# Kernel optimization log

Measured on AMD Instinct MI355X. Metric: run time of the kernel, lower is better.

Reference implementation:

```python
import jax, jax.numpy as jnp
import numpy as np

N_NODES = 50000
N_EDGES = 800000
N_FEAT = 128
N_HID = 256
N_PAIRS = 100000


def _gcn_norm(edge_index, n_nodes):
    # add self loops, compute D^-1/2 (A+I) D^-1/2 edge weights (PyG gcn_norm)
    loops = jnp.arange(n_nodes, dtype=edge_index.dtype)
    row = jnp.concatenate([edge_index[0], loops])
    col = jnp.concatenate([edge_index[1], loops])
    deg = jax.ops.segment_sum(jnp.ones_like(col, dtype=jnp.float32), col,
                              num_segments=n_nodes)
    dinv = jnp.where(deg > 0, jax.lax.rsqrt(deg), 0.0)
    norm = dinv[row] * dinv[col]  # [E + N]
    return row, col, norm


def _gcn_conv(x, W, b, row, col, norm, n_nodes):
    h = x @ W                       # [N, out]
    msg = h[row] * norm[:, None]    # gather + scale  [E+N, out]
    agg = jax.ops.segment_sum(msg, col, num_segments=n_nodes)  # scatter-add
    return agg + b


def setup_inputs() -> dict:
    key = jax.random.key(0)
    ks = jax.random.split(key, 9)
    edge_index = jax.random.randint(ks[0], (2, N_EDGES), 0, N_NODES, dtype=jnp.int64)
    features = jax.random.normal(ks[1], (N_NODES, N_FEAT), dtype=jnp.float32)
    mask = jax.random.randint(ks[2], (N_PAIRS, 2), 0, N_NODES, dtype=jnp.int64)
    s1 = 1.0 / np.sqrt(N_FEAT)
    s2 = 1.0 / np.sqrt(N_HID)
    W1 = jax.random.uniform(ks[3], (N_FEAT, N_HID), jnp.float32, -s1, s1)
    b1 = jnp.zeros((N_HID,), jnp.float32)
    W2 = jax.random.uniform(ks[4], (N_HID, N_FEAT), jnp.float32, -s2, s2)
    b2 = jnp.zeros((N_FEAT,), jnp.float32)
    Wl = jax.random.uniform(ks[5], (N_HID, 1), jnp.float32, -s2, s2)
    bl = jax.random.uniform(ks[6], (1,), jnp.float32, -s2, s2)
    return {"edge_index": edge_index, "features": features, "mask": mask,
            "W1": W1, "b1": b1, "W2": W2, "b2": b2, "Wl": Wl, "bl": bl}


def reference(edge_index, features, mask, W1, b1, W2, b2, Wl, bl):
    n = features.shape[0]
    row, col, norm = _gcn_norm(edge_index, n)
    h = _gcn_conv(features, W1, b1, row, col, norm, n)   # GCNConv a
    h = jax.nn.relu(h)                                   # dropout p=0 -> identity
    h = _gcn_conv(h, W2, b2, row, col, norm, n)          # GCNConv b
    mt = mask.T
    p1 = jax.lax.stop_gradient(h[mt[0]])                 # .detach()
    p2 = jax.lax.stop_gradient(h[mt[1]])
    hp = jnp.concatenate([p1, p2], axis=1)               # [n_pairs, 2*n_feat]
    return jax.nn.sigmoid(hp @ Wl + bl)
```

## Files before the change

### kernel.cpp

```cpp
#include <hip/hip_runtime.h>
#include <math.h>

#define NFEAT 128
#define NHID 256
#define NBLK 128

typedef __attribute__((ext_vector_type(8))) short short8;
typedef __attribute__((ext_vector_type(4))) float f32x4;

__device__ inline unsigned short f2bf(float f) {
  unsigned u = __float_as_uint(f);
  u += 0x7fffu + ((u >> 16) & 1u);
  return (unsigned short)(u >> 16);
}
__device__ inline float bflo(unsigned u) { return __uint_as_float(u << 16); }
__device__ inline float bfhi(unsigned u) { return __uint_as_float(u & 0xffff0000u); }


__device__ inline void packOne(const float* __restrict__ W,
                               unsigned short* __restrict__ Wp, int idx, int KS,
                               int OUT) {
  int lane = idx & 63;
  int t = idx >> 6;
  int ks = t % KS;
  int nt = t / KS;
  int n = nt * 16 + (lane & 15);
  int k0 = ks * 32 + (lane >> 4) * 8;
  unsigned short v[8];
#pragma unroll
  for (int j = 0; j < 8; j++) v[j] = f2bf(W[(size_t)(k0 + j) * OUT + n]);
  *reinterpret_cast<short8*>(Wp + (size_t)idx * 8) =
      *reinterpret_cast<short8*>(v);
}

__global__ __launch_bounds__(1024) void k_hist_pack(
    const int* __restrict__ col, int* __restrict__ hist2d, int nE, int nb,
    const float* __restrict__ W1, const float* __restrict__ W2,
    unsigned short* __restrict__ W1p, unsigned short* __restrict__ W2p) {
  if (blockIdx.x >= NBLK) {
    int idx = (blockIdx.x - NBLK) * 1024 + threadIdx.x;
    if (idx < 4096) packOne(W1, W1p, idx, 4, 256);
    else packOne(W2, W2p, idx - 4096, 8, 128);
    return;
  }
  __shared__ int h[1024];
  for (int i = threadIdx.x; i < nb; i += 1024) h[i] = 0;
  __syncthreads();
  int chunk = (nE + NBLK - 1) / NBLK;
  int beg = blockIdx.x * chunk, end = min(beg + chunk, nE);
  for (int e = beg + threadIdx.x; e < end; e += 1024)
    atomicAdd(&h[col[e] >> 6], 1);
  __syncthreads();
  for (int i = threadIdx.x; i < nb; i += 1024)
    hist2d[i * NBLK + blockIdx.x] = h[i];
}

__global__ __launch_bounds__(256) void k_bsum(const int* __restrict__ a,
                                              int* __restrict__ psum, int S,
                                              const float* __restrict__ b2,
                                              const float* __restrict__ Wl,
                                              const float* __restrict__ bl,
                                              float* __restrict__ Cbuf) {
  int t = threadIdx.x;
  if (blockIdx.x == gridDim.x - 1) {
    float v = (t < 128) ? b2[t] * (Wl[t] + Wl[128 + t]) : 0.f;
#pragma unroll
    for (int o = 32; o; o >>= 1) v += __shfl_down(v, o);
    __shared__ float fw[4];
    if ((t & 63) == 0) fw[t >> 6] = v;
    __syncthreads();
    if (t == 0) Cbuf[0] = fw[0] + fw[1] + fw[2] + fw[3] + bl[0];
    return;
  }
  int i = blockIdx.x * 256 + t;
  int v = (i < S) ? a[i] : 0;
#pragma unroll
  for (int o = 32; o; o >>= 1) v += __shfl_down(v, o);
  __shared__ int ws[4];
  if ((t & 63) == 0) ws[t >> 6] = v;
  __syncthreads();
  if (t == 0) psum[blockIdx.x] = ws[0] + ws[1] + ws[2] + ws[3];
}

__global__ __launch_bounds__(256) void k_s3m(const int* __restrict__ a,
                                             const int* __restrict__ psum,
                                             int* __restrict__ out, int S) {
  __shared__ int sh[256];
  __shared__ int ws[4];
  int t = threadIdx.x;
  int b = blockIdx.x;
  int partial = 0;
  for (int i = t; i < b; i += 256) partial += psum[i];
#pragma unroll
  for (int o = 32; o; o >>= 1) partial += __shfl_down(partial, o);
  if ((t & 63) == 0) ws[t >> 6] = partial;
  int i = b * 256 + t;
  int d = (i < S) ? a[i] : 0;
  sh[t] = d;
  __syncthreads();
  int base = ws[0] + ws[1] + ws[2] + ws[3];
  for (int o = 1; o < 256; o <<= 1) {
    int u = (t >= o) ? sh[t - o] : 0;
    __syncthreads();
    sh[t] += u;
    __syncthreads();
  }
  if (i < S) out[i] = base + sh[t] - d;
}

__global__ __launch_bounds__(1024) void k_part2(const int* __restrict__ row,
                                                const int* __restrict__ col,
                                                const int* __restrict__ sbase,
                                                unsigned* __restrict__ tmp,
                                                int nE, int nb) {
  __shared__ int cur[1024];
  for (int i = threadIdx.x; i < nb; i += 1024)
    cur[i] = sbase[i * NBLK + blockIdx.x];
  __syncthreads();
  int chunk = (nE + NBLK - 1) / NBLK;
  int beg = blockIdx.x * chunk, end = min(beg + chunk, nE);
  for (int e = beg + threadIdx.x; e < end; e += 1024) {
    int c = col[e];
    int pos = atomicAdd(&cur[c >> 6], 1);
    tmp[pos] = ((unsigned)(c & 63) << 16) | (unsigned)row[e];
  }
}

__global__ __launch_bounds__(256) void k_bsort_cvt(
    const unsigned* __restrict__ tmp, const int* __restrict__ sbase,
    int* __restrict__ ebuf, int* __restrict__ offs, float* __restrict__ dinv,
    const float* __restrict__ feat, unsigned short* __restrict__ xs, int n,
    int nE, int nb) {
  __shared__ int bins[64], cur[64];
  __shared__ float sdinv[64];
  int b = blockIdx.x;
  int beg = sbase[b * NBLK];
  int end = (b == nb - 1) ? nE : sbase[(b + 1) * NBLK];
  int t = threadIdx.x;
  if (t == 0 && b == nb - 1) offs[n] = nE;
  if (t < 64) bins[t] = 0;
  __syncthreads();
  for (int i = beg + t; i < end; i += 256) atomicAdd(&bins[tmp[i] >> 16], 1);
  __syncthreads();
  if (t < 64) {
    int v = bins[t];
    int s = v;
#pragma unroll
    for (int o = 1; o < 64; o <<= 1) {
      int u = __shfl_up(s, o);
      if (t >= o) s += u;
    }
    int off = beg + s - v;
    cur[t] = off;
    float dv = rsqrtf((float)(v + 1));
    sdinv[t] = dv;
    int node = b * 64 + t;
    if (node < n) {
      offs[node] = off;
      dinv[node] = dv;
    }
  }
  __syncthreads();
  for (int i = beg + t; i < end; i += 256) {
    unsigned p = tmp[i];
    int pos = atomicAdd(&cur[p >> 16], 1);
    ebuf[pos] = (int)(p & 0xffffu);
  }
  for (int i = t; i < 64 * 32; i += 256) {
    int r = i >> 5;
    int node = b * 64 + r;
    if (node >= n) break;
    float d = sdinv[r];
    float4 v = reinterpret_cast<const float4*>(feat)[(size_t)node * 32 + (i & 31)];
    unsigned short o[4] = {f2bf(v.x * d), f2bf(v.y * d), f2bf(v.z * d),
                           f2bf(v.w * d)};
    reinterpret_cast<ushort4*>(xs)[(size_t)node * 32 + (i & 31)] =
        *reinterpret_cast<ushort4*>(o);
  }
}

__global__ __launch_bounds__(256) void k_agg_bf(
    const unsigned int* __restrict__ G, const int* __restrict__ offs,
    const int* __restrict__ ebuf, const float* __restrict__ dinv,
    unsigned int* __restrict__ OUTP, int n) {
  int node = blockIdx.x * 4 + (threadIdx.x >> 6);
  if (node >= n) return;
  int lane = threadIdx.x & 63;
  int g = lane >> 4;
  int c = lane & 15;
  int beg = offs[node], end = offs[node + 1];
  float acc[8];
  if (g == 0) {
    uint4 s = *reinterpret_cast<const uint4*>(G + (size_t)node * 64 + c * 4);
    acc[0] = bflo(s.x); acc[1] = bfhi(s.x); acc[2] = bflo(s.y); acc[3] = bfhi(s.y);
    acc[4] = bflo(s.z); acc[5] = bfhi(s.z); acc[6] = bflo(s.w); acc[7] = bfhi(s.w);
  } else {
#pragma unroll
    for (int j = 0; j < 8; j++) acc[j] = 0.f;
  }
  int e = beg + g;
  for (; e + 4 < end; e += 8) {
    int i0 = ebuf[e], i1 = ebuf[e + 4];
    uint4 v0 = *reinterpret_cast<const uint4*>(G + (size_t)i0 * 64 + c * 4);
    uint4 v1 = *reinterpret_cast<const uint4*>(G + (size_t)i1 * 64 + c * 4);
    acc[0] += bflo(v0.x); acc[1] += bfhi(v0.x);
    acc[2] += bflo(v0.y); acc[3] += bfhi(v0.y);
    acc[4] += bflo(v0.z); acc[5] += bfhi(v0.z);
    acc[6] += bflo(v0.w); acc[7] += bfhi(v0.w);
    acc[0] += bflo(v1.x); acc[1] += bfhi(v1.x);
    acc[2] += bflo(v1.y); acc[3] += bfhi(v1.y);
    acc[4] += bflo(v1.z); acc[5] += bfhi(v1.z);
    acc[6] += bflo(v1.w); acc[7] += bfhi(v1.w);
  }
  if (e < end) {
    uint4 v = *reinterpret_cast<const uint4*>(G + (size_t)ebuf[e] * 64 + c * 4);
    acc[0] += bflo(v.x); acc[1] += bfhi(v.x);
    acc[2] += bflo(v.y); acc[3] += bfhi(v.y);
    acc[4] += bflo(v.z); acc[5] += bfhi(v.z);
    acc[6] += bflo(v.w); acc[7] += bfhi(v.w);
  }
#pragma unroll
  for (int j = 0; j < 8; j++) {
    acc[j] += __shfl_down(acc[j], 32);
    acc[j] += __shfl_down(acc[j], 16);
  }
  if (g == 0) {
    float d = dinv[node];
    unsigned o[4];
#pragma unroll
    for (int k = 0; k < 4; k++)
      o[k] = (unsigned)f2bf(acc[2 * k] * d) |
             ((unsigned)f2bf(acc[2 * k + 1] * d) << 16);
    *reinterpret_cast<uint4*>(OUTP + (size_t)node * 64 + c * 4) =
        *reinterpret_cast<uint4*>(o);
  }
}

__global__ __launch_bounds__(256) void k_mfma_fused(
    const unsigned short* __restrict__ A, const unsigned short* __restrict__ B1p,
    const unsigned short* __restrict__ B2p, const float* __restrict__ b1,
    const float* __restrict__ dinv, const float* __restrict__ Wl,
    float* __restrict__ P) {
  __shared__ unsigned short sh1[32 * 264];
  __shared__ float pacc[32][2];
  int rt0 = blockIdx.x * 2;
  int wave = threadIdx.x >> 6;
  int lane = threadIdx.x & 63;
  int quad = lane >> 4;
  int mrow0 = rt0 * 16 + (lane & 15);
  if (threadIdx.x < 64) pacc[threadIdx.x >> 1][threadIdx.x & 1] = 0.f;

  f32x4 acc[2][4] = {};
  const short8* Ap0 =
      reinterpret_cast<const short8*>(A + (size_t)mrow0 * NFEAT + quad * 8);
  const short8* Ap1 = reinterpret_cast<const short8*>(
      A + (size_t)(mrow0 + 16) * NFEAT + quad * 8);
#pragma unroll
  for (int ks = 0; ks < 4; ks++) {
    short8 a0 = Ap0[ks * 4];
    short8 a1 = Ap1[ks * 4];
#pragma unroll
    for (int ct = 0; ct < 4; ct++) {
      int nt = wave * 4 + ct;
      short8 b = *reinterpret_cast<const short8*>(
          B1p + ((size_t)(nt * 4 + ks) * 64 + lane) * 8);
      acc[0][ct] = __builtin_amdgcn_mfma_f32_16x16x32_bf16(a0, b, acc[0][ct], 0, 0, 0);
      acc[1][ct] = __builtin_amdgcn_mfma_f32_16x16x32_bf16(a1, b, acc[1][ct], 0, 0, 0);
    }
  }
#pragma unroll
  for (int ct = 0; ct < 4; ct++) {
    int c = (wave * 4 + ct) * 16 + (lane & 15);
    float bv = b1[c];
#pragma unroll
    for (int rg = 0; rg < 2; rg++)
#pragma unroll
      for (int i = 0; i < 4; i++) {
        float v = fmaxf(acc[rg][ct][i] + bv, 0.f);
        sh1[(rg * 16 + quad * 4 + i) * 264 + c] = f2bf(v);
      }
  }
  __syncthreads();

  f32x4 acc2[2][2] = {};
  const unsigned short* a2_0 = sh1 + (size_t)(lane & 15) * 264 + quad * 8;
  const unsigned short* a2_1 = sh1 + (size_t)(16 + (lane & 15)) * 264 + quad * 8;
#pragma unroll
  for (int ks = 0; ks < 8; ks++) {
    short8 a0 = *reinterpret_cast<const short8*>(a2_0 + ks * 32);
    short8 a1 = *reinterpret_cast<const short8*>(a2_1 + ks * 32);
#pragma unroll
    for (int ct = 0; ct < 2; ct++) {
      int nt = wave * 2 + ct;
      short8 b = *reinterpret_cast<const short8*>(
          B2p + ((size_t)(nt * 8 + ks) * 64 + lane) * 8);
      acc2[0][ct] = __builtin_amdgcn_mfma_f32_16x16x32_bf16(a0, b, acc2[0][ct], 0, 0, 0);
      acc2[1][ct] = __builtin_amdgcn_mfma_f32_16x16x32_bf16(a1, b, acc2[1][ct], 0, 0, 0);
    }
  }
  float p1[2][4] = {}, p2[2][4] = {};
#pragma unroll
  for (int rg = 0; rg < 2; rg++) {
    int r0 = (rt0 + rg) * 16 + quad * 4;
    float dv[4];
#pragma unroll
    for (int i = 0; i < 4; i++) dv[i] = dinv[r0 + i];
#pragma unroll
    for (int ct = 0; ct < 2; ct++) {
      int c = (wave * 2 + ct) * 16 + (lane & 15);
      float wl1 = Wl[c], wl2 = Wl[128 + c];
#pragma unroll
      for (int i = 0; i < 4; i++) {
        float v = acc2[rg][ct][i] * dv[i];
        p1[rg][i] = fmaf(v, wl1, p1[rg][i]);
        p2[rg][i] = fmaf(v, wl2, p2[rg][i]);
      }
    }
  }
#pragma unroll
  for (int rg = 0; rg < 2; rg++)
#pragma unroll
    for (int i = 0; i < 4; i++) {
#pragma unroll
      for (int o = 8; o; o >>= 1) {
        p1[rg][i] += __shfl_xor(p1[rg][i], o);
        p2[rg][i] += __shfl_xor(p2[rg][i], o);
      }
    }
  if ((lane & 15) == 0) {
#pragma unroll
    for (int rg = 0; rg < 2; rg++)
#pragma unroll
      for (int i = 0; i < 4; i++) {
        int row = rg * 16 + quad * 4 + i;
        atomicAdd(&pacc[row][0], p1[rg][i]);
        atomicAdd(&pacc[row][1], p2[rg][i]);
      }
  }
  __syncthreads();
  if (threadIdx.x < 64) {
    int row = threadIdx.x >> 1, comp = threadIdx.x & 1;
    P[(size_t)(rt0 * 16 + row) * 2 + comp] = pacc[row][comp];
  }
}

__global__ __launch_bounds__(256) void k_agg_s(const float2* __restrict__ p,
                                               const int* __restrict__ offs,
                                               const int* __restrict__ ebuf,
                                               const float* __restrict__ dinv,
                                               float2* __restrict__ q, int n) {
  int i = blockIdx.x * 256 + threadIdx.x;
  if (i >= n) return;
  int beg = offs[i], end = offs[i + 1];
  float2 s = p[i];
  int e = beg;
  for (; e + 4 <= end; e += 4) {
    int s0 = ebuf[e], s1 = ebuf[e + 1], s2 = ebuf[e + 2], s3 = ebuf[e + 3];
    float2 v0 = p[s0], v1 = p[s1], v2 = p[s2], v3 = p[s3];
    s.x += v0.x + v1.x + v2.x + v3.x;
    s.y += v0.y + v1.y + v2.y + v3.y;
  }
  for (; e < end; e++) {
    float2 v = p[ebuf[e]];
    s.x += v.x;
    s.y += v.y;
  }
  float d = dinv[i];
  q[i] = make_float2(s.x * d, s.y * d);
}

__global__ __launch_bounds__(256) void k_head2(const float2* __restrict__ q,
                                               const int* __restrict__ mask,
                                               const float* __restrict__ Cbuf,
                                               float* __restrict__ out, int P) {
  int p = blockIdx.x * 256 + threadIdx.x;
  if (p >= P) return;
  int m0 = mask[2 * p], m1 = mask[2 * p + 1];
  float s = q[m0].x + q[m1].y + Cbuf[0];
  out[p] = 1.0f / (1.0f + expf(-s));
}

extern "C" void kernel_launch(void* const* d_in, const int* in_sizes, int n_in,
                              void* d_out, int out_size, void* d_ws,
                              size_t ws_size, hipStream_t stream) {
  const int* edge = (const int*)d_in[0];
  const float* feat = (const float*)d_in[1];
  const int* mask = (const int*)d_in[2];
  const float* W1 = (const float*)d_in[3];
  const float* b1 = (const float*)d_in[4];
  const float* W2 = (const float*)d_in[5];
  const float* b2 = (const float*)d_in[6];
  const float* Wl = (const float*)d_in[7];
  const float* bl = (const float*)d_in[8];
  float* out = (float*)d_out;

  const int E = in_sizes[0] / 2;
  const int N = in_sizes[1] / NFEAT;
  const int P = in_sizes[2] / 2;
  const int* rowp = edge;
  const int* colp = edge + E;
  const int nrt = N / 16;
  const int nb = (N + 63) / 64;
  const int S = nb * NBLK;
  const int nS = (S + 255) / 256;

  auto aln = [](size_t x) { return (x + 255) & ~(size_t)255; };
  const size_t rowSlack = (size_t)16 * NFEAT * 2;
  char* w = (char*)d_ws;
  int* hist2d = (int*)w;           w += aln((size_t)S * 4);
  int* sbase = (int*)w;            w += aln((size_t)S * 4);
  int* psum = (int*)w;             w += aln((size_t)1024 * 4);
  float* Cbuf = (float*)w;         w += aln(256);
  int* offs = (int*)w;             w += aln((size_t)(N + 1) * 4);
  int* ebuf = (int*)w;             w += aln((size_t)E * 4);
  unsigned* tmp = (unsigned*)w;    w += aln((size_t)E * 4);
  float* dinv = (float*)w;         w += aln((size_t)N * 4 + 1024);
  unsigned short* xs = (unsigned short*)w;  w += aln((size_t)N * NFEAT * 2);
  unsigned short* z = (unsigned short*)w;   w += aln((size_t)N * NFEAT * 2 + rowSlack);
  float* p = (float*)w;            w += aln((size_t)(N + 32) * 8);
  float2* q = (float2*)w;          w += aln((size_t)N * 8);
  unsigned short* W1p = (unsigned short*)w; w += aln((size_t)NFEAT * NHID * 2);
  unsigned short* W2p = (unsigned short*)w; w += aln((size_t)NHID * NFEAT * 2);

  k_hist_pack<<<NBLK + 8, 1024, 0, stream>>>(colp, hist2d, E, nb, W1, W2, W1p,
                                             W2p);
  k_bsum<<<nS + 1, 256, 0, stream>>>(hist2d, psum, S, b2, Wl, bl, Cbuf);
  k_s3m<<<nS, 256, 0, stream>>>(hist2d, psum, sbase, S);
  k_part2<<<NBLK, 1024, 0, stream>>>(rowp, colp, sbase, tmp, E, nb);
  k_bsort_cvt<<<nb, 256, 0, stream>>>(tmp, sbase, ebuf, offs, dinv, feat, xs,
                                      N, E, nb);
  k_agg_bf<<<(N + 3) / 4, 256, 0, stream>>>((const unsigned*)xs, offs, ebuf,
                                            dinv, (unsigned*)z, N);
  k_mfma_fused<<<(nrt + 1) / 2, 256, 0, stream>>>(z, W1p, W2p, b1, dinv, Wl, p);
  k_agg_s<<<(N + 255) / 256, 256, 0, stream>>>((const float2*)p, offs, ebuf,
                                               dinv, q, N);
  k_head2<<<(P + 255) / 256, 256, 0, stream>>>(q, mask, Cbuf, out, P);
}
```

Baseline: 174.7 us.

## Slice feature matrix into column slabs for cache-friendly gather aggregation

The bf16 scaled feature matrix is stored as four 32-column slabs (slice-major), and the first aggregation kernel runs one grid per slab, so each gather touches a 64-byte row slice from a slab small enough to stay in cache. The aggregated output keeps the sliced layout, and the MFMA kernel reads its A operand from the slabs. Separately, the scalar second aggregation now uses four lanes per node with shuffle reduction instead of one thread per node, to balance degree variance. The cost is four times as many edge-index reads and more blocks, plus more shuffle reductions.

```diff
diff --git a/kernel.cpp b/kernel.cpp
--- a/kernel.cpp
+++ b/kernel.cpp
@@ -166,15 +166,18 @@
     int pos = atomicAdd(&cur[p >> 16], 1);
     ebuf[pos] = (int)(p & 0xffffu);
   }
-  for (int i = t; i < 64 * 32; i += 256) {
-    int r = i >> 5;
+  for (int i = t; i < 4 * 64 * 8; i += 256) {
+    int s = i >> 9;
+    int r = (i >> 3) & 63;
+    int ch = i & 7;
     int node = b * 64 + r;
-    if (node >= n) break;
+    if (node >= n) continue;
     float d = sdinv[r];
-    float4 v = reinterpret_cast<const float4*>(feat)[(size_t)node * 32 + (i & 31)];
+    float4 v =
+        reinterpret_cast<const float4*>(feat)[(size_t)node * 32 + s * 8 + ch];
     unsigned short o[4] = {f2bf(v.x * d), f2bf(v.y * d), f2bf(v.z * d),
                            f2bf(v.w * d)};
-    reinterpret_cast<ushort4*>(xs)[(size_t)node * 32 + (i & 31)] =
+    reinterpret_cast<ushort4*>(xs)[((size_t)s * n + node) * 8 + ch] =
         *reinterpret_cast<ushort4*>(o);
   }
 }
@@ -182,38 +185,26 @@
 __global__ __launch_bounds__(256) void k_agg_bf(
     const unsigned int* __restrict__ G, const int* __restrict__ offs,
     const int* __restrict__ ebuf, const float* __restrict__ dinv,
-    unsigned int* __restrict__ OUTP, int n) {
-  int node = blockIdx.x * 4 + (threadIdx.x >> 6);
+    unsigned int* __restrict__ OUTP, int n, int nbn, int zs) {
+  int slice = blockIdx.x / nbn;
+  int node = (blockIdx.x - slice * nbn) * 4 + (threadIdx.x >> 6);
   if (node >= n) return;
   int lane = threadIdx.x & 63;
-  int g = lane >> 4;
-  int c = lane & 15;
+  int g = lane >> 2;
+  int c = lane & 3;
   int beg = offs[node], end = offs[node + 1];
   float acc[8];
   if (g == 0) {
-    uint4 s = *reinterpret_cast<const uint4*>(G + (size_t)node * 64 + c * 4);
+    uint4 s = *reinterpret_cast<const uint4*>(G + ((size_t)slice * n + node) * 16 + c * 4);
     acc[0] = bflo(s.x); acc[1] = bfhi(s.x); acc[2] = bflo(s.y); acc[3] = bfhi(s.y);
     acc[4] = bflo(s.z); acc[5] = bfhi(s.z); acc[6] = bflo(s.w); acc[7] = bfhi(s.w);
   } else {
 #pragma unroll
     for (int j = 0; j < 8; j++) acc[j] = 0.f;
   }
-  int e = beg + g;
-  for (; e + 4 < end; e += 8) {
-    int i0 = ebuf[e], i1 = ebuf[e + 4];
-    uint4 v0 = *reinterpret_cast<const uint4*>(G + (size_t)i0 * 64 + c * 4);
-    uint4 v1 = *reinterpret_cast<const uint4*>(G + (size_t)i1 * 64 + c * 4);
-    acc[0] += bflo(v0.x); acc[1] += bfhi(v0.x);
-    acc[2] += bflo(v0.y); acc[3] += bfhi(v0.y);
-    acc[4] += bflo(v0.z); acc[5] += bfhi(v0.z);
-    acc[6] += bflo(v0.w); acc[7] += bfhi(v0.w);
-    acc[0] += bflo(v1.x); acc[1] += bfhi(v1.x);
-    acc[2] += bflo(v1.y); acc[3] += bfhi(v1.y);
-    acc[4] += bflo(v1.z); acc[5] += bfhi(v1.z);
-    acc[6] += bflo(v1.w); acc[7] += bfhi(v1.w);
-  }
-  if (e < end) {
-    uint4 v = *reinterpret_cast<const uint4*>(G + (size_t)ebuf[e] * 64 + c * 4);
+  for (int e = beg + g; e < end; e += 16) {
+    int src = ebuf[e];
+    uint4 v = *reinterpret_cast<const uint4*>(G + ((size_t)slice * n + src) * 16 + c * 4);
     acc[0] += bflo(v.x); acc[1] += bfhi(v.x);
     acc[2] += bflo(v.y); acc[3] += bfhi(v.y);
     acc[4] += bflo(v.z); acc[5] += bfhi(v.z);
@@ -223,6 +214,8 @@
   for (int j = 0; j < 8; j++) {
     acc[j] += __shfl_down(acc[j], 32);
     acc[j] += __shfl_down(acc[j], 16);
+    acc[j] += __shfl_down(acc[j], 8);
+    acc[j] += __shfl_down(acc[j], 4);
   }
   if (g == 0) {
     float d = dinv[node];
@@ -231,7 +224,7 @@
     for (int k = 0; k < 4; k++)
       o[k] = (unsigned)f2bf(acc[2 * k] * d) |
              ((unsigned)f2bf(acc[2 * k + 1] * d) << 16);
-    *reinterpret_cast<uint4*>(OUTP + (size_t)node * 64 + c * 4) =
+    *reinterpret_cast<uint4*>(OUTP + ((size_t)slice * zs + node) * 16 + c * 4) =
         *reinterpret_cast<uint4*>(o);
   }
 }
@@ -240,7 +233,7 @@
     const unsigned short* __restrict__ A, const unsigned short* __restrict__ B1p,
     const unsigned short* __restrict__ B2p, const float* __restrict__ b1,
     const float* __restrict__ dinv, const float* __restrict__ Wl,
-    float* __restrict__ P) {
+    float* __restrict__ P, int zs) {
   __shared__ unsigned short sh1[32 * 264];
   __shared__ float pacc[32][2];
   int rt0 = blockIdx.x * 2;
@@ -251,14 +244,12 @@
   if (threadIdx.x < 64) pacc[threadIdx.x >> 1][threadIdx.x & 1] = 0.f;
 
   f32x4 acc[2][4] = {};
-  const short8* Ap0 =
-      reinterpret_cast<const short8*>(A + (size_t)mrow0 * NFEAT + quad * 8);
-  const short8* Ap1 = reinterpret_cast<const short8*>(
-      A + (size_t)(mrow0 + 16) * NFEAT + quad * 8);
 #pragma unroll
   for (int ks = 0; ks < 4; ks++) {
-    short8 a0 = Ap0[ks * 4];
-    short8 a1 = Ap1[ks * 4];
+    short8 a0 = *reinterpret_cast<const short8*>(
+        A + ((size_t)ks * zs + mrow0) * 32 + quad * 8);
+    short8 a1 = *reinterpret_cast<const short8*>(
+        A + ((size_t)ks * zs + mrow0 + 16) * 32 + quad * 8);
 #pragma unroll
     for (int ct = 0; ct < 4; ct++) {
       int nt = wave * 4 + ct;
@@ -349,24 +340,25 @@
                                                const int* __restrict__ ebuf,
                                                const float* __restrict__ dinv,
                                                float2* __restrict__ q, int n) {
-  int i = blockIdx.x * 256 + threadIdx.x;
+  int i = blockIdx.x * 64 + (threadIdx.x >> 2);
   if (i >= n) return;
+  int sub = threadIdx.x & 3;
   int beg = offs[i], end = offs[i + 1];
-  float2 s = p[i];
-  int e = beg;
-  for (; e + 4 <= end; e += 4) {
-    int s0 = ebuf[e], s1 = ebuf[e + 1], s2 = ebuf[e + 2], s3 = ebuf[e + 3];
-    float2 v0 = p[s0], v1 = p[s1], v2 = p[s2], v3 = p[s3];
-    s.x += v0.x + v1.x + v2.x + v3.x;
-    s.y += v0.y + v1.y + v2.y + v3.y;
-  }
-  for (; e < end; e++) {
+  float sx = 0.f, sy = 0.f;
+  for (int e = beg + sub; e < end; e += 4) {
     float2 v = p[ebuf[e]];
-    s.x += v.x;
-    s.y += v.y;
-  }
-  float d = dinv[i];
-  q[i] = make_float2(s.x * d, s.y * d);
+    sx += v.x;
+    sy += v.y;
+  }
+  sx += __shfl_down(sx, 2);
+  sy += __shfl_down(sy, 2);
+  sx += __shfl_down(sx, 1);
+  sy += __shfl_down(sy, 1);
+  if (sub == 0) {
+    float2 self = p[i];
+    float d = dinv[i];
+    q[i] = make_float2((sx + self.x) * d, (sy + self.y) * d);
+  }
 }
 
 __global__ __launch_bounds__(256) void k_head2(const float2* __restrict__ q,
@@ -403,9 +395,10 @@
   const int nb = (N + 63) / 64;
   const int S = nb * NBLK;
   const int nS = (S + 255) / 256;
+  const int nbn = (N + 3) / 4;
+  const int ZS = N + 16;
 
   auto aln = [](size_t x) { return (x + 255) & ~(size_t)255; };
-  const size_t rowSlack = (size_t)16 * NFEAT * 2;
   char* w = (char*)d_ws;
   int* hist2d = (int*)w;           w += aln((size_t)S * 4);
   int* sbase = (int*)w;            w += aln((size_t)S * 4);
@@ -416,7 +409,7 @@
   unsigned* tmp = (unsigned*)w;    w += aln((size_t)E * 4);
   float* dinv = (float*)w;         w += aln((size_t)N * 4 + 1024);
   unsigned short* xs = (unsigned short*)w;  w += aln((size_t)N * NFEAT * 2);
-  unsigned short* z = (unsigned short*)w;   w += aln((size_t)N * NFEAT * 2 + rowSlack);
+  unsigned short* z = (unsigned short*)w;   w += aln((size_t)4 * ZS * 32 * 2);
   float* p = (float*)w;            w += aln((size_t)(N + 32) * 8);
   float2* q = (float2*)w;          w += aln((size_t)N * 8);
   unsigned short* W1p = (unsigned short*)w; w += aln((size_t)NFEAT * NHID * 2);
@@ -429,10 +422,11 @@
   k_part2<<<NBLK, 1024, 0, stream>>>(rowp, colp, sbase, tmp, E, nb);
   k_bsort_cvt<<<nb, 256, 0, stream>>>(tmp, sbase, ebuf, offs, dinv, feat, xs,
                                       N, E, nb);
-  k_agg_bf<<<(N + 3) / 4, 256, 0, stream>>>((const unsigned*)xs, offs, ebuf,
-                                            dinv, (unsigned*)z, N);
-  k_mfma_fused<<<(nrt + 1) / 2, 256, 0, stream>>>(z, W1p, W2p, b1, dinv, Wl, p);
-  k_agg_s<<<(N + 255) / 256, 256, 0, stream>>>((const float2*)p, offs, ebuf,
-                                               dinv, q, N);
+  k_agg_bf<<<4 * nbn, 256, 0, stream>>>((const unsigned*)xs, offs, ebuf, dinv,
+                                        (unsigned*)z, N, nbn, ZS);
+  k_mfma_fused<<<(nrt + 1) / 2, 256, 0, stream>>>(z, W1p, W2p, b1, dinv, Wl, p,
+                                                  ZS);
+  k_agg_s<<<(N + 63) / 64, 256, 0, stream>>>((const float2*)p, offs, ebuf,
+                                             dinv, q, N);
   k_head2<<<(P + 255) / 256, 256, 0, stream>>>(q, mask, Cbuf, out, P);
 }
```

After: 214.2 us. 1.23x slower.

## Replace two-level bucket sort CSR build with global-atomic degree count and fill

Applied to the files above, without the earlier changes.

The CSR construction changes from a block-histogram, partition and in-bucket sort pipeline to a per-node degree count with global atomics. A scan then produces offsets with the self loop placed as each node's first neighbor, and an atomic fill writes the remaining neighbors, which removes one pass over the edges and the tmp buffer. Feature conversion to bf16 is merged into the fill kernel. The aggregation kernels now get the self loop from the edge list and use byte-address indexing, and the second aggregation splits each node across 4 lanes. Neighbor order is now nondeterministic and may be less local, and global atomic contention replaces LDS atomics.

```diff
diff --git a/kernel.cpp b/kernel.cpp
--- a/kernel.cpp
+++ b/kernel.cpp
@@ -3,10 +3,10 @@
 
 #define NFEAT 128
 #define NHID 256
-#define NBLK 128
 
 typedef __attribute__((ext_vector_type(8))) short short8;
 typedef __attribute__((ext_vector_type(4))) float f32x4;
+typedef __attribute__((ext_vector_type(2))) float f32x2;
 
 __device__ inline unsigned short f2bf(float f) {
   unsigned u = __float_as_uint(f);
@@ -15,7 +15,6 @@
 }
 __device__ inline float bflo(unsigned u) { return __uint_as_float(u << 16); }
 __device__ inline float bfhi(unsigned u) { return __uint_as_float(u & 0xffff0000u); }
-
 
 __device__ inline void packOne(const float* __restrict__ W,
                                unsigned short* __restrict__ Wp, int idx, int KS,
@@ -33,26 +32,18 @@
       *reinterpret_cast<short8*>(v);
 }
 
-__global__ __launch_bounds__(1024) void k_hist_pack(
-    const int* __restrict__ col, int* __restrict__ hist2d, int nE, int nb,
+__global__ __launch_bounds__(256) void k_deg_pack(
+    const int* __restrict__ col, int* __restrict__ deg, int nE, int nEB,
     const float* __restrict__ W1, const float* __restrict__ W2,
     unsigned short* __restrict__ W1p, unsigned short* __restrict__ W2p) {
-  if (blockIdx.x >= NBLK) {
-    int idx = (blockIdx.x - NBLK) * 1024 + threadIdx.x;
+  if (blockIdx.x >= nEB) {
+    int idx = (blockIdx.x - nEB) * 256 + threadIdx.x;
     if (idx < 4096) packOne(W1, W1p, idx, 4, 256);
     else packOne(W2, W2p, idx - 4096, 8, 128);
     return;
   }
-  __shared__ int h[1024];
-  for (int i = threadIdx.x; i < nb; i += 1024) h[i] = 0;
-  __syncthreads();
-  int chunk = (nE + NBLK - 1) / NBLK;
-  int beg = blockIdx.x * chunk, end = min(beg + chunk, nE);
-  for (int e = beg + threadIdx.x; e < end; e += 1024)
-    atomicAdd(&h[col[e] >> 6], 1);
-  __syncthreads();
-  for (int i = threadIdx.x; i < nb; i += 1024)
-    hist2d[i * NBLK + blockIdx.x] = h[i];
+  int i = blockIdx.x * 256 + threadIdx.x;
+  if (i < nE) atomicAdd(&deg[col[i]], 1);
 }
 
 __global__ __launch_bounds__(256) void k_bsum(const int* __restrict__ a,
@@ -73,7 +64,7 @@
     return;
   }
   int i = blockIdx.x * 256 + t;
-  int v = (i < S) ? a[i] : 0;
+  int v = (i < S) ? a[i] + 1 : 0;
 #pragma unroll
   for (int o = 32; o; o >>= 1) v += __shfl_down(v, o);
   __shared__ int ws[4];
@@ -82,9 +73,12 @@
   if (t == 0) psum[blockIdx.x] = ws[0] + ws[1] + ws[2] + ws[3];
 }
 
-__global__ __launch_bounds__(256) void k_s3m(const int* __restrict__ a,
-                                             const int* __restrict__ psum,
-                                             int* __restrict__ out, int S) {
+__global__ __launch_bounds__(256) void k_scan(const int* __restrict__ deg,
+                                              const int* __restrict__ psum,
+                                              int* __restrict__ offs,
+                                              int* __restrict__ cur,
+                                              float* __restrict__ dinv,
+                                              int* __restrict__ ebuf, int n) {
   __shared__ int sh[256];
   __shared__ int ws[4];
   int t = threadIdx.x;
@@ -95,7 +89,7 @@
   for (int o = 32; o; o >>= 1) partial += __shfl_down(partial, o);
   if ((t & 63) == 0) ws[t >> 6] = partial;
   int i = b * 256 + t;
-  int d = (i < S) ? a[i] : 0;
+  int d = (i < n) ? deg[i] + 1 : 0;
   sh[t] = d;
   __syncthreads();
   int base = ws[0] + ws[1] + ws[2] + ws[3];
@@ -105,133 +99,85 @@
     sh[t] += u;
     __syncthreads();
   }
-  if (i < S) out[i] = base + sh[t] - d;
-}
-
-__global__ __launch_bounds__(1024) void k_part2(const int* __restrict__ row,
-                                                const int* __restrict__ col,
-                                                const int* __restrict__ sbase,
-                                                unsigned* __restrict__ tmp,
-                                                int nE, int nb) {
-  __shared__ int cur[1024];
-  for (int i = threadIdx.x; i < nb; i += 1024)
-    cur[i] = sbase[i * NBLK + blockIdx.x];
-  __syncthreads();
-  int chunk = (nE + NBLK - 1) / NBLK;
-  int beg = blockIdx.x * chunk, end = min(beg + chunk, nE);
-  for (int e = beg + threadIdx.x; e < end; e += 1024) {
-    int c = col[e];
-    int pos = atomicAdd(&cur[c >> 6], 1);
-    tmp[pos] = ((unsigned)(c & 63) << 16) | (unsigned)row[e];
-  }
-}
-
-__global__ __launch_bounds__(256) void k_bsort_cvt(
-    const unsigned* __restrict__ tmp, const int* __restrict__ sbase,
-    int* __restrict__ ebuf, int* __restrict__ offs, float* __restrict__ dinv,
-    const float* __restrict__ feat, unsigned short* __restrict__ xs, int n,
-    int nE, int nb) {
-  __shared__ int bins[64], cur[64];
-  __shared__ float sdinv[64];
-  int b = blockIdx.x;
-  int beg = sbase[b * NBLK];
-  int end = (b == nb - 1) ? nE : sbase[(b + 1) * NBLK];
-  int t = threadIdx.x;
-  if (t == 0 && b == nb - 1) offs[n] = nE;
-  if (t < 64) bins[t] = 0;
-  __syncthreads();
-  for (int i = beg + t; i < end; i += 256) atomicAdd(&bins[tmp[i] >> 16], 1);
-  __syncthreads();
-  if (t < 64) {
-    int v = bins[t];
-    int s = v;
-#pragma unroll
-    for (int o = 1; o < 64; o <<= 1) {
-      int u = __shfl_up(s, o);
-      if (t >= o) s += u;
-    }
-    int off = beg + s - v;
-    cur[t] = off;
-    float dv = rsqrtf((float)(v + 1));
-    sdinv[t] = dv;
-    int node = b * 64 + t;
-    if (node < n) {
-      offs[node] = off;
-      dinv[node] = dv;
-    }
-  }
-  __syncthreads();
-  for (int i = beg + t; i < end; i += 256) {
-    unsigned p = tmp[i];
-    int pos = atomicAdd(&cur[p >> 16], 1);
-    ebuf[pos] = (int)(p & 0xffffu);
-  }
-  for (int i = t; i < 64 * 32; i += 256) {
-    int r = i >> 5;
-    int node = b * 64 + r;
-    if (node >= n) break;
-    float d = sdinv[r];
-    float4 v = reinterpret_cast<const float4*>(feat)[(size_t)node * 32 + (i & 31)];
+  if (i < n) {
+    int off = base + sh[t] - d;
+    offs[i] = off;
+    cur[i] = off + 1;
+    dinv[i] = rsqrtf((float)d);
+    ebuf[off] = i;
+    if (i == n - 1) offs[n] = off + d;
+  }
+}
+
+__global__ __launch_bounds__(256) void k_fill_cvt(
+    const int* __restrict__ row, const int* __restrict__ col,
+    int* __restrict__ cur, int* __restrict__ ebuf,
+    const float* __restrict__ feat, const float* __restrict__ dinv,
+    unsigned short* __restrict__ xs, int nE, int nItems) {
+  int i = blockIdx.x * 256 + threadIdx.x;
+  if (i < nE) {
+    int c = col[i];
+    int pos = atomicAdd(&cur[c], 1);
+    ebuf[pos] = row[i];
+  }
+  if (i < nItems) {
+    int node = i >> 5;
+    float d = dinv[node];
+    float4 v = reinterpret_cast<const float4*>(feat)[(size_t)i];
     unsigned short o[4] = {f2bf(v.x * d), f2bf(v.y * d), f2bf(v.z * d),
                            f2bf(v.w * d)};
-    reinterpret_cast<ushort4*>(xs)[(size_t)node * 32 + (i & 31)] =
-        *reinterpret_cast<ushort4*>(o);
+    reinterpret_cast<ushort4*>(xs)[(size_t)i] = *reinterpret_cast<ushort4*>(o);
   }
 }
 
 __global__ __launch_bounds__(256) void k_agg_bf(
-    const unsigned int* __restrict__ G, const int* __restrict__ offs,
+    const char* __restrict__ Gb, const int* __restrict__ offs,
     const int* __restrict__ ebuf, const float* __restrict__ dinv,
-    unsigned int* __restrict__ OUTP, int n) {
+    char* __restrict__ Ob, int n) {
   int node = blockIdx.x * 4 + (threadIdx.x >> 6);
   if (node >= n) return;
   int lane = threadIdx.x & 63;
   int g = lane >> 4;
-  int c = lane & 15;
+  unsigned cb = (unsigned)(lane & 15) << 4;
   int beg = offs[node], end = offs[node + 1];
-  float acc[8];
-  if (g == 0) {
-    uint4 s = *reinterpret_cast<const uint4*>(G + (size_t)node * 64 + c * 4);
-    acc[0] = bflo(s.x); acc[1] = bfhi(s.x); acc[2] = bflo(s.y); acc[3] = bfhi(s.y);
-    acc[4] = bflo(s.z); acc[5] = bfhi(s.z); acc[6] = bflo(s.w); acc[7] = bfhi(s.w);
-  } else {
-#pragma unroll
-    for (int j = 0; j < 8; j++) acc[j] = 0.f;
-  }
+  f32x2 acc[4] = {};
   int e = beg + g;
   for (; e + 4 < end; e += 8) {
     int i0 = ebuf[e], i1 = ebuf[e + 4];
-    uint4 v0 = *reinterpret_cast<const uint4*>(G + (size_t)i0 * 64 + c * 4);
-    uint4 v1 = *reinterpret_cast<const uint4*>(G + (size_t)i1 * 64 + c * 4);
-    acc[0] += bflo(v0.x); acc[1] += bfhi(v0.x);
-    acc[2] += bflo(v0.y); acc[3] += bfhi(v0.y);
-    acc[4] += bflo(v0.z); acc[5] += bfhi(v0.z);
-    acc[6] += bflo(v0.w); acc[7] += bfhi(v0.w);
-    acc[0] += bflo(v1.x); acc[1] += bfhi(v1.x);
-    acc[2] += bflo(v1.y); acc[3] += bfhi(v1.y);
-    acc[4] += bflo(v1.z); acc[5] += bfhi(v1.z);
-    acc[6] += bflo(v1.w); acc[7] += bfhi(v1.w);
+    uint4 v0 = *reinterpret_cast<const uint4*>(Gb + (((unsigned)i0 << 8) | cb));
+    uint4 v1 = *reinterpret_cast<const uint4*>(Gb + (((unsigned)i1 << 8) | cb));
+    acc[0] += (f32x2){bflo(v0.x), bfhi(v0.x)};
+    acc[1] += (f32x2){bflo(v0.y), bfhi(v0.y)};
+    acc[2] += (f32x2){bflo(v0.z), bfhi(v0.z)};
+    acc[3] += (f32x2){bflo(v0.w), bfhi(v0.w)};
+    acc[0] += (f32x2){bflo(v1.x), bfhi(v1.x)};
+    acc[1] += (f32x2){bflo(v1.y), bfhi(v1.y)};
+    acc[2] += (f32x2){bflo(v1.z), bfhi(v1.z)};
+    acc[3] += (f32x2){bflo(v1.w), bfhi(v1.w)};
   }
   if (e < end) {
-    uint4 v = *reinterpret_cast<const uint4*>(G + (size_t)ebuf[e] * 64 + c * 4);
-    acc[0] += bflo(v.x); acc[1] += bfhi(v.x);
-    acc[2] += bflo(v.y); acc[3] += bfhi(v.y);
-    acc[4] += bflo(v.z); acc[5] += bfhi(v.z);
-    acc[6] += bflo(v.w); acc[7] += bfhi(v.w);
-  }
-#pragma unroll
-  for (int j = 0; j < 8; j++) {
-    acc[j] += __shfl_down(acc[j], 32);
-    acc[j] += __shfl_down(acc[j], 16);
+    int i0 = ebuf[e];
+    uint4 v0 = *reinterpret_cast<const uint4*>(Gb + (((unsigned)i0 << 8) | cb));
+    acc[0] += (f32x2){bflo(v0.x), bfhi(v0.x)};
+    acc[1] += (f32x2){bflo(v0.y), bfhi(v0.y)};
+    acc[2] += (f32x2){bflo(v0.z), bfhi(v0.z)};
+    acc[3] += (f32x2){bflo(v0.w), bfhi(v0.w)};
+  }
+#pragma unroll
+  for (int j = 0; j < 4; j++) {
+    acc[j].x += __shfl_down(acc[j].x, 32);
+    acc[j].y += __shfl_down(acc[j].y, 32);
+    acc[j].x += __shfl_down(acc[j].x, 16);
+    acc[j].y += __shfl_down(acc[j].y, 16);
   }
   if (g == 0) {
     float d = dinv[node];
     unsigned o[4];
 #pragma unroll
     for (int k = 0; k < 4; k++)
-      o[k] = (unsigned)f2bf(acc[2 * k] * d) |
-             ((unsigned)f2bf(acc[2 * k + 1] * d) << 16);
-    *reinterpret_cast<uint4*>(OUTP + (size_t)node * 64 + c * 4) =
+      o[k] = (unsigned)f2bf(acc[k].x * d) |
+             ((unsigned)f2bf(acc[k].y * d) << 16);
+    *reinterpret_cast<uint4*>(Ob + (((unsigned)node << 8) | cb)) =
         *reinterpret_cast<uint4*>(o);
   }
 }
@@ -349,24 +295,24 @@
                                                const int* __restrict__ ebuf,
                                                const float* __restrict__ dinv,
                                                float2* __restrict__ q, int n) {
-  int i = blockIdx.x * 256 + threadIdx.x;
+  int i = blockIdx.x * 64 + (threadIdx.x >> 2);
   if (i >= n) return;
+  int sub = threadIdx.x & 3;
   int beg = offs[i], end = offs[i + 1];
-  float2 s = p[i];
-  int e = beg;
-  for (; e + 4 <= end; e += 4) {
-    int s0 = ebuf[e], s1 = ebuf[e + 1], s2 = ebuf[e + 2], s3 = ebuf[e + 3];
-    float2 v0 = p[s0], v1 = p[s1], v2 = p[s2], v3 = p[s3];
-    s.x += v0.x + v1.x + v2.x + v3.x;
-    s.y += v0.y + v1.y + v2.y + v3.y;
-  }
-  for (; e < end; e++) {
+  float sx = 0.f, sy = 0.f;
+  for (int e = beg + sub; e < end; e += 4) {
     float2 v = p[ebuf[e]];
-    s.x += v.x;
-    s.y += v.y;
-  }
-  float d = dinv[i];
-  q[i] = make_float2(s.x * d, s.y * d);
+    sx += v.x;
+    sy += v.y;
+  }
+  sx += __shfl_down(sx, 2);
+  sy += __shfl_down(sy, 2);
+  sx += __shfl_down(sx, 1);
+  sy += __shfl_down(sy, 1);
+  if (sub == 0) {
+    float d = dinv[i];
+    q[i] = make_float2(sx * d, sy * d);
+  }
 }
 
 __global__ __launch_bounds__(256) void k_head2(const float2* __restrict__ q,
@@ -400,20 +346,20 @@
   const int* rowp = edge;
   const int* colp = edge + E;
   const int nrt = N / 16;
-  const int nb = (N + 63) / 64;
-  const int S = nb * NBLK;
-  const int nS = (S + 255) / 256;
+  const int nS = (N + 255) / 256;
+  const int nEB = (E + 255) / 256;
+  const int nItems = N * (NFEAT / 4);
+  const int nFC = max(nEB, (nItems + 255) / 256);
 
   auto aln = [](size_t x) { return (x + 255) & ~(size_t)255; };
   const size_t rowSlack = (size_t)16 * NFEAT * 2;
   char* w = (char*)d_ws;
-  int* hist2d = (int*)w;           w += aln((size_t)S * 4);
-  int* sbase = (int*)w;            w += aln((size_t)S * 4);
+  int* deg = (int*)w;              w += aln((size_t)N * 4);
+  int* cur = (int*)w;              w += aln((size_t)N * 4);
   int* psum = (int*)w;             w += aln((size_t)1024 * 4);
   float* Cbuf = (float*)w;         w += aln(256);
   int* offs = (int*)w;             w += aln((size_t)(N + 1) * 4);
-  int* ebuf = (int*)w;             w += aln((size_t)E * 4);
-  unsigned* tmp = (unsigned*)w;    w += aln((size_t)E * 4);
+  int* ebuf = (int*)w;             w += aln((size_t)(E + N) * 4);
   float* dinv = (float*)w;         w += aln((size_t)N * 4 + 1024);
   unsigned short* xs = (unsigned short*)w;  w += aln((size_t)N * NFEAT * 2);
   unsigned short* z = (unsigned short*)w;   w += aln((size_t)N * NFEAT * 2 + rowSlack);
@@ -422,17 +368,17 @@
   unsigned short* W1p = (unsigned short*)w; w += aln((size_t)NFEAT * NHID * 2);
   unsigned short* W2p = (unsigned short*)w; w += aln((size_t)NHID * NFEAT * 2);
 
-  k_hist_pack<<<NBLK + 8, 1024, 0, stream>>>(colp, hist2d, E, nb, W1, W2, W1p,
-                                             W2p);
-  k_bsum<<<nS + 1, 256, 0, stream>>>(hist2d, psum, S, b2, Wl, bl, Cbuf);
-  k_s3m<<<nS, 256, 0, stream>>>(hist2d, psum, sbase, S);
-  k_part2<<<NBLK, 1024, 0, stream>>>(rowp, colp, sbase, tmp, E, nb);
-  k_bsort_cvt<<<nb, 256, 0, stream>>>(tmp, sbase, ebuf, offs, dinv, feat, xs,
-                                      N, E, nb);
-  k_agg_bf<<<(N + 3) / 4, 256, 0, stream>>>((const unsigned*)xs, offs, ebuf,
-                                            dinv, (unsigned*)z, N);
+  hipMemsetAsync(deg, 0, (size_t)N * 4, stream);
+  k_deg_pack<<<nEB + 32, 256, 0, stream>>>(colp, deg, E, nEB, W1, W2, W1p,
+                                           W2p);
+  k_bsum<<<nS + 1, 256, 0, stream>>>(deg, psum, N, b2, Wl, bl, Cbuf);
+  k_scan<<<nS, 256, 0, stream>>>(deg, psum, offs, cur, dinv, ebuf, N);
+  k_fill_cvt<<<nFC, 256, 0, stream>>>(rowp, colp, cur, ebuf, feat, dinv, xs, E,
+                                      nItems);
+  k_agg_bf<<<(N + 3) / 4, 256, 0, stream>>>((const char*)xs, offs, ebuf, dinv,
+                                            (char*)z, N);
   k_mfma_fused<<<(nrt + 1) / 2, 256, 0, stream>>>(z, W1p, W2p, b1, dinv, Wl, p);
-  k_agg_s<<<(N + 255) / 256, 256, 0, stream>>>((const float2*)p, offs, ebuf,
-                                               dinv, q, N);
+  k_agg_s<<<(N + 63) / 64, 256, 0, stream>>>((const float2*)p, offs, ebuf,
+                                             dinv, q, N);
   k_head2<<<(P + 255) / 256, 256, 0, stream>>>(q, mask, Cbuf, out, P);
 }
```

After: 231.8 us. 1.33x slower.
